# Kernel optimization log

Hardware: AMD Instinct MI355X
Metric: run time of the kernel (lower is better)

## Reference

```python
import jax, jax.numpy as jnp
import numpy as np

NUM_HEADS = 16
HIDDEN = 1024
HEAD_DIM = HIDDEN // NUM_HEADS


def setup_inputs() -> dict:
    key = jax.random.key(0)
    ks = jax.random.split(key, 9)
    B, S, D = 2, 2048, HIDDEN
    s = 1.0 / np.sqrt(D)
    return {
        "x": jax.random.normal(ks[0], (B, S, D), dtype=jnp.float32),
        "Wq": jax.random.normal(ks[1], (D, D), dtype=jnp.float32) * s,
        "bq": jnp.zeros((D,), dtype=jnp.float32),
        "Wk": jax.random.normal(ks[2], (D, D), dtype=jnp.float32) * s,
        "bk": jnp.zeros((D,), dtype=jnp.float32),
        "Wv": jax.random.normal(ks[3], (D, D), dtype=jnp.float32) * s,
        "bv": jnp.zeros((D,), dtype=jnp.float32),
        "Wo": jax.random.normal(ks[4], (D, D), dtype=jnp.float32) * s,
        "bo": jnp.zeros((D,), dtype=jnp.float32),
    }


def reference(x, Wq, bq, Wk, bk, Wv, bv, Wo, bo):
    B, S, D = x.shape
    H, Hd = NUM_HEADS, HEAD_DIM
    # projections -> [B, H, S, Hd]
    def proj(W, b):
        return (x @ W + b).reshape(B, S, H, Hd).transpose(0, 2, 1, 3)
    q = proj(Wq, bq)
    k = proj(Wk, bk)
    v = proj(Wv, bv)
    scores = jnp.einsum('bhqd,bhkd->bhqk', q, k) / jnp.sqrt(jnp.float32(Hd))
    p_attn = jax.nn.softmax(scores, axis=-1)  # dropout = identity (eval)
    ctx = jnp.einsum('bhqk,bhkd->bhqd', p_attn, v)
    attn_mean = jnp.mean(p_attn, axis=1)  # [B, S, S]
    out = ctx.transpose(0, 2, 1, 3).reshape(B, S, D) @ Wo + bo
    return out, attn_mean
```

## Files before the change

### kernel.cpp

```cpp
#include <hip/hip_runtime.h>
#include <math.h>

#define NUM_HEADS 16
#define HEAD_DIM  64
#define HIDDEN    1024
#define BATCH     2
#define SEQ       2048

#define QSCALE 0.1803368801111204f

typedef short bf16x8 __attribute__((ext_vector_type(8)));
typedef short short4v __attribute__((ext_vector_type(4)));
typedef float f32x4 __attribute__((ext_vector_type(4)));

#if __has_builtin(__builtin_amdgcn_exp2f)
#define EXP2F __builtin_amdgcn_exp2f
#else
#define EXP2F exp2f
#endif

#define ACQB(N) do { asm volatile("s_waitcnt vmcnt(" #N ")" ::: "memory"); \
                     __builtin_amdgcn_s_barrier(); } while (0)
#define RELB()  do { asm volatile("s_waitcnt lgkmcnt(0)" ::: "memory");   \
                     __builtin_amdgcn_sched_barrier(0);                    \
                     __builtin_amdgcn_s_barrier(); } while (0)

__device__ __forceinline__ short f2bf(float f) {
    union { float f; unsigned int u; } x; x.f = f;
    unsigned int r = x.u + 0x7fffu + ((x.u >> 16) & 1u);
    return (short)(r >> 16);
}

__device__ __forceinline__ unsigned int pack_bf16_trunc(float lo, float hi) {
    return __builtin_amdgcn_perm(__float_as_uint(hi), __float_as_uint(lo), 0x07060302u);
}

__device__ __forceinline__ void async16(const void* g, void* l) {
    __builtin_amdgcn_global_load_lds(
        (const __attribute__((address_space(1))) void*)g,
        (__attribute__((address_space(3))) void*)l, 16, 0, 0);
}

__global__ __launch_bounds__(256)
void prep_kernel(const float* __restrict__ x,
                 const float* __restrict__ Wq, const float* __restrict__ Wk,
                 const float* __restrict__ Wv, const float* __restrict__ Wo,
                 short* __restrict__ xb, short* __restrict__ Wt4)
{
    __shared__ float t[64][65];
    const int tid = threadIdx.x;
    const int bid = blockIdx.x;
    if (bid < 4096) {
        size_t i = ((size_t)bid * 256 + tid) * 4;
        float4 v = *(const float4*)&x[i];
        short4v o;
        o.x = f2bf(v.x); o.y = f2bf(v.y); o.z = f2bf(v.z); o.w = f2bf(v.w);
        *(short4v*)&xb[i] = o;
        return;
    }
    const int tb = bid - 4096;
    const int z  = tb >> 8;
    const int cx = tb & 15, cy = (tb >> 4) & 15;
    const float* W = (z == 0) ? Wq : (z == 1) ? Wk : (z == 2) ? Wv : Wo;
    short* dst = Wt4 + (size_t)z * HIDDEN * HIDDEN;
    const int c0 = cx * 64;
    const int r0 = cy * 64;
    const int cl = tid & 63, rw = tid >> 6;
    #pragma unroll
    for (int p = 0; p < 16; ++p) {
        int row = p * 4 + rw;
        t[row][cl] = W[(size_t)(r0 + row) * HIDDEN + c0 + cl];
    }
    __syncthreads();
    #pragma unroll
    for (int p = 0; p < 16; ++p) {
        int orow = p * 4 + rw;
        dst[(size_t)(c0 + orow) * HIDDEN + r0 + cl] = f2bf(t[cl][orow]);
    }
}

__global__ __launch_bounds__(256)
void qkv_proj_kernel(const short* __restrict__ xb, const short* __restrict__ Wt4,
                     const float* __restrict__ bq, const float* __restrict__ bk,
                     const float* __restrict__ bv,
                     short* __restrict__ Qb, short* __restrict__ Kb,
                     short* __restrict__ Vt)
{
    __shared__ short ldsA[128 * 64];
    __shared__ short ldsB[128 * 64];
    const int tid = threadIdx.x;
    const int lane = tid & 63, w = tid >> 6;
    const int l = lane & 15, q = lane >> 4;
    const int lin = blockIdx.y * 8 + blockIdx.x;
    const int cid = (lin & 7) * 32 + (lin >> 3);
    const int n0 = (cid & 7) * 128;
    const int m0 = (cid >> 3) * 128;
    const int z  = blockIdx.z;
    const short* Wt = Wt4 + (size_t)z * HIDDEN * HIDDEN;
    const int wm = (w >> 1) * 64, wn = (w & 1) * 64;
    const int sw = l & 7;

    const short* pa[4]; const short* pb[4]; int ldst[4];
    #pragma unroll
    for (int hh = 0; hh < 4; ++hh) {
        int c = hh * 256 + tid;
        int row = c >> 3;
        int kcg = (c & 7) ^ (row & 7);
        pa[hh] = xb + (size_t)(m0 + row) * HIDDEN + kcg * 8;
        pb[hh] = Wt + (size_t)(n0 + row) * HIDDEN + kcg * 8;
        ldst[hh] = c * 8;
    }

    f32x4 acc[4][4];
    #pragma unroll
    for (int i = 0; i < 4; ++i)
        #pragma unroll
        for (int j = 0; j < 4; ++j)
            acc[i][j] = (f32x4){0.f, 0.f, 0.f, 0.f};

    auto STG = [&]() {
        #pragma unroll
        for (int hh = 0; hh < 4; ++hh) {
            async16(pa[hh], &ldsA[ldst[hh]]);
            async16(pb[hh], &ldsB[ldst[hh]]);
            pa[hh] += 64; pb[hh] += 64;
        }
    };

    STG();
    ACQB(0);
    for (int t = 0; t < 16; ++t) {
        bf16x8 af[4][2], bfr[4][2];
        #pragma unroll
        for (int kk = 0; kk < 2; ++kk) {
            const int cc = ((4 * kk + q) ^ sw) * 8;
            #pragma unroll
            for (int i = 0; i < 4; ++i)
                af[i][kk] = *(const bf16x8*)&ldsA[(wm + 16 * i + l) * 64 + cc];
            #pragma unroll
            for (int j = 0; j < 4; ++j)
                bfr[j][kk] = *(const bf16x8*)&ldsB[(wn + 16 * j + l) * 64 + cc];
        }
        RELB();
        if (t < 15) STG();
        __builtin_amdgcn_s_setprio(1);
        #pragma unroll
        for (int kk = 0; kk < 2; ++kk)
            #pragma unroll
            for (int i = 0; i < 4; ++i)
                #pragma unroll
                for (int j = 0; j < 4; ++j)
                    acc[i][j] = __builtin_amdgcn_mfma_f32_16x16x32_bf16(
                        af[i][kk], bfr[j][kk], acc[i][j], 0, 0, 0);
        __builtin_amdgcn_s_setprio(0);
        if (t < 15) ACQB(0);
    }

    const float* bias = (z == 0) ? bq : (z == 1) ? bk : bv;
    const float sc = (z == 0) ? QSCALE : 1.0f;
    if (z < 2) {
        short* Ob = (z == 0) ? Qb : Kb;
        #pragma unroll
        for (int j = 0; j < 4; ++j) {
            int n = n0 + wn + 16 * j + l;
            float bval = bias[n];
            int h = n >> 6, hd = n & 63;
            #pragma unroll
            for (int i = 0; i < 4; ++i) {
                #pragma unroll
                for (int reg = 0; reg < 4; ++reg) {
                    int m = m0 + wm + 16 * i + 4 * q + reg;
                    int b_ = m >> 11, s = m & 2047;
                    Ob[(((size_t)(b_ * NUM_HEADS + h) * SEQ) + s) * HEAD_DIM + hd] =
                        f2bf((acc[i][j][reg] + bval) * sc);
                }
            }
        }
    } else {
        #pragma unroll
        for (int j = 0; j < 4; ++j) {
            int n = n0 + wn + 16 * j + l;
            float bval = bias[n];
            int h = n >> 6, hd = n & 63;
            #pragma unroll
            for (int i = 0; i < 4; ++i) {
                int mb = m0 + wm + 16 * i + 4 * q;
                int b_ = mb >> 11, s = mb & 2047;
                short4v pk;
                #pragma unroll
                for (int reg = 0; reg < 4; ++reg)
                    pk[reg] = f2bf(acc[i][j][reg] + bval);
                *(short4v*)&Vt[(((size_t)(b_ * NUM_HEADS + h) * HEAD_DIM) + hd) * SEQ + s] = pk;
            }
        }
    }
}

__global__ __launch_bounds__(512, 4)
void flash_kernel(const short* __restrict__ Qb, const short* __restrict__ Kb,
                  const short* __restrict__ Vt, short* __restrict__ Cb,
                  float* __restrict__ Lb)
{
    __shared__ __align__(16) char fsm[35840];
    short (*Ks)[64 * 64] = (short (*)[64 * 64])fsm;
    short (*Vs)[64 * 64] = (short (*)[64 * 64])(fsm + 16384);
    float (*Xch)[64][35] = (float (*)[64][35])fsm;

    const int tid = threadIdx.x, lane = tid & 63, w = tid >> 6;
    const int l = lane & 15, q = lane >> 4;
    const int qg = w & 3;
    const int kh = w >> 2;
    const int bid = blockIdx.x;
    const int xcd = bid & 7, j = bid >> 3;
    const int h  = xcd + 8 * (j & 1);
    const int b  = (j >> 1) & 1;
    const int q0 = (j >> 2) * 128;
    const int Q0 = q0 + qg * 32;
    const size_t base  = (size_t)(b * NUM_HEADS + h) * SEQ * HEAD_DIM;
    const size_t vbase = (size_t)(b * NUM_HEADS + h) * HEAD_DIM * SEQ;

    bf16x8 bq[2][2];
    #pragma unroll
    for (int u = 0; u < 2; ++u)
        #pragma unroll
        for (int ks = 0; ks < 2; ++ks)
            bq[u][ks] = *(const bf16x8*)(Qb + base +
                (size_t)(Q0 + 16 * u + l) * HEAD_DIM + 32 * ks + 8 * q);

    const int c = tid;
    const int row = c >> 3;
    const int g = ((c & 7) ^ (row & 7)) * 8;
    const short* kp = Kb + base + (size_t)row * HEAD_DIM + g;
    const short* vp = Vt + vbase + (size_t)row * SEQ + g;

    const int sw = l & 7;
    int kaddr[2];
    #pragma unroll
    for (int ks = 0; ks < 2; ++ks)
        kaddr[ks] = (32 * kh + l) * 64 + ((4 * ks + q) ^ sw) * 8;
    const int vc0 = 4 * kh + (q >> 1);
    const int vaddr0 = l * 64 + ((vc0      ^ sw) * 8) + 4 * (q & 1);
    const int vaddr1 = l * 64 + (((vc0 + 2) ^ sw) * 8) + 4 * (q & 1);

    f32x4 ctx[2][4];
    #pragma unroll
    for (int u = 0; u < 2; ++u)
        #pragma unroll
        for (int m = 0; m < 4; ++m) ctx[u][m] = (f32x4){0.f, 0.f, 0.f, 0.f};
    float l_part[2] = {0.f, 0.f};

    auto STG = [&](int buf) {
        async16(kp, &Ks[buf][c * 8]);
        async16(vp, &Vs[buf][c * 8]);
        kp += 64 * HEAD_DIM;
        vp += 64;
    };
    auto CMP = [&](int buf) {
        f32x4 st[2][2];
        #pragma unroll
        for (int u = 0; u < 2; ++u)
            #pragma unroll
            for (int t = 0; t < 2; ++t) st[u][t] = (f32x4){0.f, 0.f, 0.f, 0.f};
        __builtin_amdgcn_s_setprio(1);
        #pragma unroll
        for (int ks = 0; ks < 2; ++ks) {
            #pragma unroll
            for (int t = 0; t < 2; ++t) {
                bf16x8 ak = *(const bf16x8*)&Ks[buf][kaddr[ks] + t * 1024];
                st[0][t] = __builtin_amdgcn_mfma_f32_16x16x32_bf16(ak, bq[0][ks], st[0][t], 0, 0, 0);
                st[1][t] = __builtin_amdgcn_mfma_f32_16x16x32_bf16(ak, bq[1][ks], st[1][t], 0, 0, 0);
            }
        }
        __builtin_amdgcn_s_setprio(0);
        union { unsigned int u32[4]; bf16x8 v; } bp[2];
        #pragma unroll
        for (int u = 0; u < 2; ++u) {
            #pragma unroll
            for (int t = 0; t < 2; ++t) {
                float p0 = EXP2F(st[u][t][0]);
                float p1 = EXP2F(st[u][t][1]);
                float p2 = EXP2F(st[u][t][2]);
                float p3 = EXP2F(st[u][t][3]);
                l_part[u] += (p0 + p1) + (p2 + p3);
                bp[u].u32[2 * t]     = pack_bf16_trunc(p0, p1);
                bp[u].u32[2 * t + 1] = pack_bf16_trunc(p2, p3);
            }
        }
        __builtin_amdgcn_s_setprio(1);
        #pragma unroll
        for (int m = 0; m < 4; ++m) {
            short4v g0 = *(const short4v*)&Vs[buf][vaddr0 + m * 1024];
            short4v g1 = *(const short4v*)&Vs[buf][vaddr1 + m * 1024];
            bf16x8 av = __builtin_shufflevector(g0, g1, 0, 1, 2, 3, 4, 5, 6, 7);
            ctx[0][m] = __builtin_amdgcn_mfma_f32_16x16x32_bf16(av, bp[0].v, ctx[0][m], 0, 0, 0);
            ctx[1][m] = __builtin_amdgcn_mfma_f32_16x16x32_bf16(av, bp[1].v, ctx[1][m], 0, 0, 0);
        }
        __builtin_amdgcn_s_setprio(0);
    };

    STG(0); STG(1);
    ACQB(2);
    for (int tp = 0; tp < 15; ++tp) {
        CMP(0); RELB(); STG(0); ACQB(2);
        CMP(1); RELB(); STG(1); ACQB(2);
    }
    CMP(0); RELB(); ACQB(0);
    CMP(1);

    __syncthreads();

    if (kh == 1) {
        float* dst = &Xch[qg][lane][0];
        #pragma unroll
        for (int u = 0; u < 2; ++u)
            #pragma unroll
            for (int m = 0; m < 4; ++m)
                #pragma unroll
                for (int r = 0; r < 4; ++r)
                    dst[u * 16 + m * 4 + r] = ctx[u][m][r];
        dst[32] = l_part[0];
        dst[33] = l_part[1];
    }
    __syncthreads();
    if (kh == 0) {
        const float* src = &Xch[qg][lane][0];
        #pragma unroll
        for (int u = 0; u < 2; ++u)
            #pragma unroll
            for (int m = 0; m < 4; ++m)
                #pragma unroll
                for (int r = 0; r < 4; ++r)
                    ctx[u][m][r] += src[u * 16 + m * 4 + r];

        #pragma unroll
        for (int u = 0; u < 2; ++u) {
            float rs = l_part[u] + src[32 + u];
            rs += __shfl_xor(rs, 16);
            rs += __shfl_xor(rs, 32);
            float inv_l = 1.0f / rs;
            int s = Q0 + 16 * u + l;
            #pragma unroll
            for (int t = 0; t < 4; ++t) {
                short4v pk;
                #pragma unroll
                for (int reg = 0; reg < 4; ++reg)
                    pk[reg] = f2bf(ctx[u][t][reg] * inv_l);
                *(short4v*)&Cb[(((size_t)(b * NUM_HEADS + h) * SEQ) + s) * HEAD_DIM + 16 * t + 4 * q] = pk;
            }
            if (q == 0)
                Lb[(size_t)(b * NUM_HEADS + h) * SEQ + s] = inv_l;
        }
    }
}

__global__ __launch_bounds__(256)
void tail_kernel(const short* __restrict__ Cb, const short* __restrict__ Wot,
                 const float* __restrict__ bo, float* __restrict__ out,
                 const short* __restrict__ Qb, const short* __restrict__ Kb,
                 const float* __restrict__ Lb, float* __restrict__ amean)
{
    __shared__ __align__(16) short smem[24576];
    const int tid = threadIdx.x, lane = tid & 63, w = tid >> 6;
    const int l = lane & 15, q = lane >> 4;
    const int sw = l & 7;
    const int bid = blockIdx.x;
    const int xcd = bid & 7, j = bid >> 3;
    const int r3 = j % 3, j3 = j / 3;

    if (r3 == 2) {
        short (*ldsA)[64 * 64]  = (short (*)[64 * 64])smem;
        short (*ldsB)[128 * 64] = (short (*)[128 * 64])(smem + 8192);
        const int n0 = xcd * 128;
        const int m0 = j3 * 64;

        const short* pa[2]; const short* pb[4]; int lda[2], ldb[4];
        #pragma unroll
        for (int hh = 0; hh < 2; ++hh) {
            int cc = hh * 256 + tid;
            int rowc = cc >> 3;
            int kcg = (cc & 7) ^ (rowc & 7);
            int m = m0 + rowc;
            int b_ = m >> 11, s = m & 2047;
            pa[hh] = Cb + (((size_t)(b_ * NUM_HEADS) * SEQ) + s) * HEAD_DIM + kcg * 8;
            lda[hh] = cc * 8;
        }
        #pragma unroll
        for (int hh = 0; hh < 4; ++hh) {
            int cc = hh * 256 + tid;
            int rowc = cc >> 3;
            int kcg = (cc & 7) ^ (rowc & 7);
            pb[hh] = Wot + (size_t)(n0 + rowc) * HIDDEN + kcg * 8;
            ldb[hh] = cc * 8;
        }

        f32x4 acc[4][2];
        #pragma unroll
        for (int i = 0; i < 4; ++i)
            #pragma unroll
            for (int jj = 0; jj < 2; ++jj)
                acc[i][jj] = (f32x4){0.f, 0.f, 0.f, 0.f};

        auto STG = [&](int buf) {
            #pragma unroll
            for (int hh = 0; hh < 2; ++hh) {
                async16(pa[hh], &ldsA[buf][lda[hh]]);
                pa[hh] += (size_t)SEQ * HEAD_DIM;
            }
            #pragma unroll
            for (int hh = 0; hh < 4; ++hh) {
                async16(pb[hh], &ldsB[buf][ldb[hh]]);
                pb[hh] += 64;
            }
        };
        auto CMP = [&](int buf) {
            #pragma unroll
            for (int kk = 0; kk < 2; ++kk) {
                const int cc = ((4 * kk + q) ^ sw) * 8;
                bf16x8 af[4], bfr[2];
                #pragma unroll
                for (int i = 0; i < 4; ++i)
                    af[i] = *(const bf16x8*)&ldsA[buf][(16 * i + l) * 64 + cc];
                #pragma unroll
                for (int jj = 0; jj < 2; ++jj)
                    bfr[jj] = *(const bf16x8*)&ldsB[buf][(32 * w + 16 * jj + l) * 64 + cc];
                __builtin_amdgcn_s_setprio(1);
                #pragma unroll
                for (int i = 0; i < 4; ++i)
                    #pragma unroll
                    for (int jj = 0; jj < 2; ++jj)
                        acc[i][jj] = __builtin_amdgcn_mfma_f32_16x16x32_bf16(
                            af[i], bfr[jj], acc[i][jj], 0, 0, 0);
                __builtin_amdgcn_s_setprio(0);
            }
        };

        STG(0);
        for (int t = 0; t < 15; ++t) {
            STG((t & 1) ^ 1);
            ACQB(6);
            CMP(t & 1);
            RELB();
        }
        ACQB(0);
        CMP(1);

        #pragma unroll
        for (int jj = 0; jj < 2; ++jj) {
            int n = n0 + 32 * w + 16 * jj + l;
            float bval = bo[n];
            #pragma unroll
            for (int i = 0; i < 4; ++i)
                #pragma unroll
                for (int reg = 0; reg < 4; ++reg) {
                    int m = m0 + 16 * i + 4 * q + reg;
                    out[(size_t)m * HIDDEN + n] = acc[i][jj][reg] + bval;
                }
        }
    } else {
        short (*Qs)[64 * 64]  = (short (*)[64 * 64])smem;
        short (*Ks)[128 * 64] = (short (*)[128 * 64])(smem + 8192);
        const int k0 = xcd * 256 + r3 * 128;
        const int b  = j3 & 1;
        const int q0 = (j3 >> 1) * 64;
        const size_t HSTRIDE = (size_t)SEQ * HEAD_DIM;

        const short* qp[2];
        const short* kp[4];
        {
            const size_t base0 = (size_t)(b * NUM_HEADS) * HSTRIDE;
            #pragma unroll
            for (int i = 0; i < 2; ++i) {
                int cc = 256 * i + tid;
                int rowc = cc >> 3;
                int gg = ((cc & 7) ^ (rowc & 7)) * 8;
                qp[i] = Qb + base0 + (size_t)(q0 + rowc) * HEAD_DIM + gg;
            }
            #pragma unroll
            for (int i = 0; i < 4; ++i) {
                int cc = 256 * i + tid;
                int rowc = cc >> 3;
                int gg = ((cc & 7) ^ (rowc & 7)) * 8;
                kp[i] = Kb + base0 + (size_t)(k0 + rowc) * HEAD_DIM + gg;
            }
        }

        f32x4 macc[2][4];
        #pragma unroll
        for (int tk = 0; tk < 2; ++tk)
            #pragma unroll
            for (int tq = 0; tq < 4; ++tq)
                macc[tk][tq] = (f32x4){0.f, 0.f, 0.f, 0.f};

        auto STG = [&](int buf) {
            #pragma unroll
            for (int i = 0; i < 2; ++i) { async16(qp[i], &Qs[buf][(256 * i + tid) * 8]); qp[i] += HSTRIDE; }
            #pragma unroll
            for (int i = 0; i < 4; ++i) { async16(kp[i], &Ks[buf][(256 * i + tid) * 8]); kp[i] += HSTRIDE; }
        };
        int hc = 0;
        auto CMP = [&](int buf) {
            int h = hc++;
            float linv[4];
            #pragma unroll
            for (int tq = 0; tq < 4; ++tq)
                linv[tq] = Lb[(size_t)(b * NUM_HEADS + h) * SEQ + q0 + 16 * tq + l];

            bf16x8 bq[4][2], ak[2][2];
            #pragma unroll
            for (int ks = 0; ks < 2; ++ks) {
                const int cc = ((4 * ks + q) ^ sw) * 8;
                #pragma unroll
                for (int tq = 0; tq < 4; ++tq)
                    bq[tq][ks] = *(const bf16x8*)&Qs[buf][(16 * tq + l) * 64 + cc];
                #pragma unroll
                for (int tk = 0; tk < 2; ++tk)
                    ak[tk][ks] = *(const bf16x8*)&Ks[buf][(32 * w + 16 * tk + l) * 64 + cc];
            }
            #pragma unroll
            for (int tk = 0; tk < 2; ++tk) {
                #pragma unroll
                for (int tq = 0; tq < 4; ++tq) {
                    f32x4 st = (f32x4){0.f, 0.f, 0.f, 0.f};
                    st = __builtin_amdgcn_mfma_f32_16x16x32_bf16(ak[tk][0], bq[tq][0], st, 0, 0, 0);
                    st = __builtin_amdgcn_mfma_f32_16x16x32_bf16(ak[tk][1], bq[tq][1], st, 0, 0, 0);
                    float li = linv[tq];
                    #pragma unroll
                    for (int reg = 0; reg < 4; ++reg)
                        macc[tk][tq][reg] += EXP2F(st[reg]) * li;
                }
            }
        };

        STG(0); STG(1);
        ACQB(6);
        for (int tp = 0; tp < 7; ++tp) {
            CMP(0); RELB(); STG(0); ACQB(6);
            CMP(1); RELB(); STG(1); ACQB(6);
        }
        CMP(0); RELB(); ACQB(0);
        CMP(1);

        const float inv_h = 1.0f / (float)NUM_HEADS;
        #pragma unroll
        for (int tq = 0; tq < 4; ++tq) {
            int row_q = q0 + 16 * tq + l;
            #pragma unroll
            for (int tk = 0; tk < 2; ++tk) {
                int col_k = k0 + 32 * w + 16 * tk + 4 * q;
                f32x4 o;
                #pragma unroll
                for (int reg = 0; reg < 4; ++reg) o[reg] = macc[tk][tq][reg] * inv_h;
                *(f32x4*)&amean[((size_t)b * SEQ + row_q) * SEQ + col_k] = o;
            }
        }
    }
}

extern "C" void kernel_launch(void* const* d_in, const int* in_sizes, int n_in,
                              void* d_out, int out_size, void* d_ws, size_t ws_size,
                              hipStream_t stream)
{
    const float* x  = (const float*)d_in[0];
    const float* Wq = (const float*)d_in[1];
    const float* bq = (const float*)d_in[2];
    const float* Wk = (const float*)d_in[3];
    const float* bk = (const float*)d_in[4];
    const float* Wv = (const float*)d_in[5];
    const float* bv = (const float*)d_in[6];
    const float* Wo = (const float*)d_in[7];
    const float* bo = (const float*)d_in[8];

    float* out   = (float*)d_out;
    float* amean = out + (size_t)BATCH * SEQ * HIDDEN;

    const size_t NELEM = (size_t)BATCH * NUM_HEADS * SEQ * HEAD_DIM;
    short* ws  = (short*)d_ws;
    short* xb  = ws;
    short* Wt4 = xb + NELEM;
    short* Qb  = Wt4 + 4 * (size_t)HIDDEN * HIDDEN;
    short* Kb  = Qb + NELEM;
    short* Vt  = Kb + NELEM;
    short* Cb  = Vt + NELEM;
    float* Lb  = (float*)(Cb + NELEM);

    dim3 blk(256);
    prep_kernel<<<dim3(4096 + 1024), blk, 0, stream>>>(x, Wq, Wk, Wv, Wo, xb, Wt4);
    qkv_proj_kernel<<<dim3(8, 32, 3), blk, 0, stream>>>(xb, Wt4, bq, bk, bv, Qb, Kb, Vt);
    flash_kernel<<<dim3(512), dim3(512), 0, stream>>>(Qb, Kb, Vt, Cb, Lb);
    tail_kernel<<<dim3(1536), blk, 0, stream>>>(Cb, Wt4 + 3 * (size_t)HIDDEN * HIDDEN, bo, out,
                                                Qb, Kb, Lb, amean);
}
```

Measured before the change: 232.8 us.

## Remap flash/tail block indexing and stage softmax normalizers into LDS

The flash kernel now uses a plain 3D grid (q-tile, head, batch) in place of the XCD-aware swizzle of a 1D block index. The tail kernel re-derives its GEMM tile and attention-mean tile coordinates from a new block ordering. The attention-mean path now loads all 16 heads' inverse row sums for its query tile into shared memory with one async load, so each head iteration no longer does a scattered global read. These mappings change which blocks share K/V and weight data on each XCD's L2, which may hurt or help cache locality.

```diff
diff --git a/kernel.cpp b/kernel.cpp
--- a/kernel.cpp
+++ b/kernel.cpp
@@ -210,12 +210,9 @@
     const int l = lane & 15, q = lane >> 4;
     const int qg = w & 3;
     const int kh = w >> 2;
-    const int bid = blockIdx.x;
-    const int xcd = bid & 7, j = bid >> 3;
-    const int h  = xcd + 8 * (j & 1);
-    const int b  = (j >> 1) & 1;
-    const int q0 = (j >> 2) * 128;
+    const int q0 = blockIdx.x * 128;
     const int Q0 = q0 + qg * 32;
+    const int h = blockIdx.y, b = blockIdx.z;
     const size_t base  = (size_t)(b * NUM_HEADS + h) * SEQ * HEAD_DIM;
     const size_t vbase = (size_t)(b * NUM_HEADS + h) * HEAD_DIM * SEQ;
 
@@ -233,7 +230,7 @@
     const short* kp = Kb + base + (size_t)row * HEAD_DIM + g;
     const short* vp = Vt + vbase + (size_t)row * SEQ + g;
 
-    const int sw = l & 7;
+    const int sw = l & 15 & 7;
     int kaddr[2];
     #pragma unroll
     for (int ks = 0; ks < 2; ++ks)
@@ -359,19 +356,19 @@
                  const short* __restrict__ Qb, const short* __restrict__ Kb,
                  const float* __restrict__ Lb, float* __restrict__ amean)
 {
-    __shared__ __align__(16) short smem[24576];
+    __shared__ __align__(16) short smem[26624];
     const int tid = threadIdx.x, lane = tid & 63, w = tid >> 6;
     const int l = lane & 15, q = lane >> 4;
     const int sw = l & 7;
     const int bid = blockIdx.x;
-    const int xcd = bid & 7, j = bid >> 3;
-    const int r3 = j % 3, j3 = j / 3;
+    const int r3 = bid % 3, g3 = bid / 3;
 
     if (r3 == 2) {
         short (*ldsA)[64 * 64]  = (short (*)[64 * 64])smem;
         short (*ldsB)[128 * 64] = (short (*)[128 * 64])(smem + 8192);
-        const int n0 = xcd * 128;
-        const int m0 = j3 * 64;
+        const int cid = (g3 & 7) * 64 + (g3 >> 3);
+        const int n0 = (cid & 7) * 128;
+        const int m0 = (cid >> 3) * 64;
 
         const short* pa[2]; const short* pb[4]; int lda[2], ldb[4];
         #pragma unroll
@@ -459,9 +456,12 @@
     } else {
         short (*Qs)[64 * 64]  = (short (*)[64 * 64])smem;
         short (*Ks)[128 * 64] = (short (*)[128 * 64])(smem + 8192);
-        const int k0 = xcd * 256 + r3 * 128;
-        const int b  = j3 & 1;
-        const int q0 = (j3 >> 1) * 64;
+        float* Ls = (float*)(smem + 24576);
+        const int a  = g3 * 2 + r3;
+        const int k0 = (a & 15) * 128;
+        const int qy = (a >> 4) & 31;
+        const int q0 = qy * 64;
+        const int b  = a >> 9;
         const size_t HSTRIDE = (size_t)SEQ * HEAD_DIM;
 
         const short* qp[2];
@@ -503,7 +503,7 @@
             float linv[4];
             #pragma unroll
             for (int tq = 0; tq < 4; ++tq)
-                linv[tq] = Lb[(size_t)(b * NUM_HEADS + h) * SEQ + q0 + 16 * tq + l];
+                linv[tq] = Ls[h * 64 + 16 * tq + l];
 
             bf16x8 bq[4][2], ak[2][2];
             #pragma unroll
@@ -531,6 +531,11 @@
             }
         };
 
+        {
+            int hh = tid >> 4, cc = tid & 15;
+            async16(Lb + ((size_t)(b * NUM_HEADS) + hh) * SEQ + q0 + cc * 4,
+                    &Ls[hh * 64 + cc * 4]);
+        }
         STG(0); STG(1);
         ACQB(6);
         for (int tp = 0; tp < 7; ++tp) {
@@ -586,7 +591,7 @@
     dim3 blk(256);
     prep_kernel<<<dim3(4096 + 1024), blk, 0, stream>>>(x, Wq, Wk, Wv, Wo, xb, Wt4);
     qkv_proj_kernel<<<dim3(8, 32, 3), blk, 0, stream>>>(xb, Wt4, bq, bk, bv, Qb, Kb, Vt);
-    flash_kernel<<<dim3(512), dim3(512), 0, stream>>>(Qb, Kb, Vt, Cb, Lb);
+    flash_kernel<<<dim3(SEQ / 128, NUM_HEADS, BATCH), dim3(512), 0, stream>>>(Qb, Kb, Vt, Cb, Lb);
     tail_kernel<<<dim3(1536), blk, 0, stream>>>(Cb, Wt4 + 3 * (size_t)HIDDEN * HIDDEN, bo, out,
                                                 Qb, Kb, Lb, amean);
 }
```

Result: faster. 219.5 us (-5.7%).
